# Kernel tuning notes

Hardware: AMD Instinct MI355X
Metric: run time of the kernel (lower is better)

The kernel has to match this reference:

```python
import jax, jax.numpy as jnp
import numpy as np

H, W, C, SEQ = 512, 512, 64, 32


def _mask(shape, i, j):
    m = np.zeros(shape, np.float32)
    m[i, j, :, 0] = 1.0
    return jnp.asarray(m)

# directional single-tap masks matching kernel_switch_dic
MASK_RIGHT = _mask((1, 3, C, 1), 0, 0)  # out[j] <- in[j-1]
MASK_LEFT  = _mask((1, 3, C, 1), 0, 2)  # out[j] <- in[j+1]
MASK_DOWN  = _mask((3, 1, C, 1), 0, 0)  # out[i] <- in[i-1]
MASK_UP    = _mask((3, 1, C, 1), 2, 0)  # out[i] <- in[i+1]


def _shift_right(t):  # t: (H, W, C)
    return jnp.pad(t, ((0, 0), (1, 0), (0, 0)))[:, :-1, :]

def _shift_left(t):
    return jnp.pad(t, ((0, 0), (0, 1), (0, 0)))[:, 1:, :]

def _shift_down(t):
    return jnp.pad(t, ((1, 0), (0, 0), (0, 0)))[:-1, :, :]

def _shift_up(t):
    return jnp.pad(t, ((0, 1), (0, 0), (0, 0)))[1:, :, :]


def _dir_scan(img, w, shift_fn):
    # tensor_{i+1} = relu(shift(tensor_i) * w_c); res = img + sum_i tensor_i
    def step(carry, _):
        t, res = carry
        t = jax.nn.relu(shift_fn(t) * w)
        return (t, res + t), None
    (_, res), _ = jax.lax.scan(step, (img, img), None, length=SEQ)
    return res


def setup_inputs() -> dict:
    key = jax.random.key(0)
    ks = jax.random.split(key, 5)
    s = 0.05  # random_uniform default range
    return {
        "x": jax.random.normal(ks[0], (1, H, W, C), jnp.float32),
        "k_right": jax.random.uniform(ks[1], (1, 3, C, 1), jnp.float32, -s, s),
        "k_left":  jax.random.uniform(ks[2], (1, 3, C, 1), jnp.float32, -s, s),
        "k_down":  jax.random.uniform(ks[3], (3, 1, C, 1), jnp.float32, -s, s),
        "k_up":    jax.random.uniform(ks[4], (3, 1, C, 1), jnp.float32, -s, s),
    }


def reference(x, k_right, k_left, k_down, k_up):
    img = x[0]  # (H, W, C); layer only supports batch 1
    dirs = [
        (k_right, MASK_RIGHT, _shift_right),
        (k_left,  MASK_LEFT,  _shift_left),
        (k_down,  MASK_DOWN,  _shift_down),
        (k_up,    MASK_UP,    _shift_up),
    ]
    outs = []
    for k, mask, shift_fn in dirs:
        # masked depthwise kernel has a single active tap -> per-channel scalar
        w = jnp.sum(k * mask, axis=(0, 1))[:, 0]  # (C,)
        outs.append(_dir_scan(img, w, shift_fn))
    return jnp.concatenate(outs, axis=-1)[None]  # (1, H, W, 4*C)
```

## Files before the change

### kernel.cpp

```cpp
#include <hip/hip_runtime.h>


#define HH 512
#define WW 512
#define CC 64
#define CHUNK 64
#define HALO 6
#define NCH (WW / CHUNK)

template<int PASS>
__global__ __launch_bounds__(256) void spatial_rnn_pass(
    const float* __restrict__ x,
    const float* __restrict__ kA,
    const float* __restrict__ kB,
    float* __restrict__ out)
{
    const int tid = threadIdx.x;
    const int c   = tid & 63;
    const int wv  = blockIdx.x * 4 + (tid >> 6);

    const float wA = kA[c];
    const float wB = kB[2 * CC + c];
    const float wpA = fmaxf(wA, 0.0f);
    const float wpB = fmaxf(wB, 0.0f);

    long ix0, oA0;
    int dxi, dout, chunk;
    if (PASS == 0) {
        const int line = wv >> 3;
        chunk = wv & 7;
        const int p0 = chunk * CHUNK;
        ix0 = (long)line * (WW * CC) + (long)p0 * CC + c;            dxi  = CC;
        oA0 = (long)line * (WW * 4 * CC) + (long)p0 * (4 * CC) + c;
        dout = 4 * CC;
    } else {
        const int col = wv & 511;
        chunk = wv >> 9;
        const int p0 = chunk * CHUNK;
        ix0 = (long)p0 * (WW * CC) + (long)col * CC + c;             dxi  = WW * CC;
        oA0 = (long)p0 * (WW * 4 * CC) + (long)col * (4 * CC) + 2 * CC + c;
        dout = WW * 4 * CC;
    }

    float xv[CHUNK];
    #pragma unroll
    for (int t = 0; t < CHUNK; ++t)
        xv[t] = x[ix0 + (long)t * dxi];

    float rA = 0.0f;
    if (chunk != 0) {
        float hv[HALO];
        #pragma unroll
        for (int t = 0; t < HALO; ++t)
            hv[t] = x[ix0 - (long)(HALO - t) * dxi];
        #pragma unroll
        for (int t = 0; t < HALO; ++t)
            rA = fmaxf(wA * hv[t], 0.0f) + wpA * rA;
    }

    float rB = 0.0f;
    if (chunk != NCH - 1) {
        float hv[HALO];
        #pragma unroll
        for (int t = 0; t < HALO; ++t)
            hv[t] = x[ix0 + (long)(CHUNK + HALO - 1 - t) * dxi];
        #pragma unroll
        for (int t = 0; t < HALO; ++t)
            rB = fmaxf(wB * hv[t], 0.0f) + wpB * rB;
    }

    #pragma unroll
    for (int t = 0; t < CHUNK; ++t) {
        __builtin_nontemporal_store(xv[t] + rA, &out[oA0 + (long)t * dout]);
        rA = fmaxf(wA * xv[t], 0.0f) + wpA * rA;
    }
    #pragma unroll
    for (int t = CHUNK - 1; t >= 0; --t) {
        __builtin_nontemporal_store(xv[t] + rB, &out[oA0 + CC + (long)t * dout]);
        rB = fmaxf(wB * xv[t], 0.0f) + wpB * rB;
    }
}

extern "C" void kernel_launch(void* const* d_in, const int* in_sizes, int n_in,
                              void* d_out, int out_size, void* d_ws, size_t ws_size,
                              hipStream_t stream) {
    const float* x  = (const float*)d_in[0];
    const float* kr = (const float*)d_in[1];
    const float* kl = (const float*)d_in[2];
    const float* kd = (const float*)d_in[3];
    const float* ku = (const float*)d_in[4];
    float* out = (float*)d_out;

    spatial_rnn_pass<0><<<1024, 256, 0, stream>>>(x, kr, kl, out);
    spatial_rnn_pass<1><<<1024, 256, 0, stream>>>(x, kd, ku, out);
}
```

Baseline: 322.6 us.

## Fuse horizontal and vertical passes into one tile-interleaved kernel launch

```diff
diff --git a/kernel.cpp b/kernel.cpp
--- a/kernel.cpp
+++ b/kernel.cpp
@@ -8,39 +8,49 @@
 #define HALO 6
 #define NCH (WW / CHUNK)
 
-template<int PASS>
-__global__ __launch_bounds__(256) void spatial_rnn_pass(
+__global__ __launch_bounds__(256) void spatial_rnn_kernel(
     const float* __restrict__ x,
-    const float* __restrict__ kA,
-    const float* __restrict__ kB,
+    const float* __restrict__ kr,
+    const float* __restrict__ kl,
+    const float* __restrict__ kd,
+    const float* __restrict__ ku,
     float* __restrict__ out)
 {
     const int tid = threadIdx.x;
     const int c   = tid & 63;
-    const int wv  = blockIdx.x * 4 + (tid >> 6);
+    const int wv  = tid >> 6;
 
-    const float wA = kA[c];
-    const float wB = kB[2 * CC + c];
-    const float wpA = fmaxf(wA, 0.0f);
-    const float wpB = fmaxf(wB, 0.0f);
+    const int g   = blockIdx.x;
+    const int J   = g & 7;
+    const int q   = g >> 3;
+    const int I   = q >> 5;
+    const int s   = q & 31;
+    const int ln  = (s >> 1) * 4 + wv;
 
+    float wA, wB;
     long ix0, oA0;
     int dxi, dout, chunk;
-    if (PASS == 0) {
-        const int line = wv >> 3;
-        chunk = wv & 7;
+    if ((s & 1) == 0) {
+        const int row = I * 64 + ln;
+        chunk = J;
         const int p0 = chunk * CHUNK;
-        ix0 = (long)line * (WW * CC) + (long)p0 * CC + c;            dxi  = CC;
-        oA0 = (long)line * (WW * 4 * CC) + (long)p0 * (4 * CC) + c;
+        wA = kr[c];
+        wB = kl[2 * CC + c];
+        ix0 = (long)row * (WW * CC) + (long)p0 * CC + c;            dxi  = CC;
+        oA0 = (long)row * (WW * 4 * CC) + (long)p0 * (4 * CC) + c;
         dout = 4 * CC;
     } else {
-        const int col = wv & 511;
-        chunk = wv >> 9;
+        const int col = J * 64 + ln;
+        chunk = I;
         const int p0 = chunk * CHUNK;
-        ix0 = (long)p0 * (WW * CC) + (long)col * CC + c;             dxi  = WW * CC;
+        wA = kd[c];
+        wB = ku[2 * CC + c];
+        ix0 = (long)p0 * (WW * CC) + (long)col * CC + c;            dxi  = WW * CC;
         oA0 = (long)p0 * (WW * 4 * CC) + (long)col * (4 * CC) + 2 * CC + c;
         dout = WW * 4 * CC;
     }
+    const float wpA = fmaxf(wA, 0.0f);
+    const float wpB = fmaxf(wB, 0.0f);
 
     float xv[CHUNK];
     #pragma unroll
@@ -91,6 +101,5 @@
     const float* ku = (const float*)d_in[4];
     float* out = (float*)d_out;
 
-    spatial_rnn_pass<0><<<1024, 256, 0, stream>>>(x, kr, kl, out);
-    spatial_rnn_pass<1><<<1024, 256, 0, stream>>>(x, kd, ku, out);
+    spatial_rnn_kernel<<<2048, 256, 0, stream>>>(x, kr, kl, kd, ku, out);
 }
```

Result: no change. 319.2 us (-1.1%).
